# Performance work log

Hardware: AMD Instinct MI355X
Metric: run time of the kernel (lower is better)

Reference implementation:

```python
import jax, jax.numpy as jnp
import numpy as np

N, T, P = 8192, 2048, 24  # batch of series, time steps, seasonal period


def setup_inputs() -> dict:
    key = jax.random.key(0)
    k1, k2, k3, k4, k5, k6, k7 = jax.random.split(key, 7)
    return {
        "temp": jax.random.normal(k1, (N, T), dtype=jnp.float32),
        "alpha": jax.random.uniform(k2, (1,), dtype=jnp.float32),
        "beta": jax.random.uniform(k3, (1,), dtype=jnp.float32),
        "gamma": jax.random.uniform(k4, (1,), dtype=jnp.float32),
        "L0": jax.random.normal(k5, (N,), dtype=jnp.float32),
        "b0": jax.random.normal(k6, (N,), dtype=jnp.float32),
        "S0": jax.random.normal(k7, (N, P), dtype=jnp.float32),
        "seasonp": P,
    }


def reference(temp, alpha, beta, gamma, L0, b0, S0, seasonp):
    # Holt-Winters exponential smoothing recurrence (add trend), batched over N series.
    a, bt, g = alpha[0], beta[0], gamma[0]
    Tn = temp.shape[1]
    phases = jnp.arange(1, Tn, dtype=jnp.int32) % seasonp  # i % seasonp
    xs = temp[:, 1:].T  # [T-1, N]

    def step(carry, inp):
        L, b, buf = carry          # L,b: [N]; buf: [N, P] rolling seasonal buffer
        x, ph = inp
        s_read = buf[:, ph]        # S[i % seasonp] (most recent value at this phase)
        Ln = a * (x - s_read) + (1.0 - a) * (L + b)
        bn = bt * (Ln - L) + (1.0 - bt) * b
        sn = g * (x - Ln) + (1.0 - g) * s_read
        buf = buf.at[:, ph].set(sn)
        return (Ln, bn, buf), (Ln, bn, sn)

    (_, _, _), (Ls, bs, Ss) = jax.lax.scan(step, (L0, b0, S0), (xs, phases))
    L = jnp.concatenate([L0[:, None], Ls.T], axis=1)   # [N, T]
    b = jnp.concatenate([b0[:, None], bs.T], axis=1)   # [N, T]
    S = jnp.concatenate([S0[:, 0:1], Ss.T], axis=1)    # [N, T]
    return (L + b) * S
```

## Files before the change

kernel.cpp:

```cpp
#include <hip/hip_runtime.h>


typedef float f32x4 __attribute__((ext_vector_type(4)));

#define ALOAD(DST, PTR, OFF) \
  asm volatile("global_load_dwordx4 %0, %1, off offset:" #OFF \
               : "=v"(DST) : "v"(PTR));

#define ASTORE(PTR, VAL) \
  asm volatile("global_store_dwordx4 %0, %1, off" :: "v"(PTR), "v"(VAL));

#define WAITVM(N) \
  { asm volatile("s_waitcnt vmcnt(" #N ")" ::: "memory"); \
    __builtin_amdgcn_sched_barrier(0); }

__global__ __launch_bounds__(64, 1) void hw_kernel(
    const float* __restrict__ temp,
    const float* __restrict__ alpha,
    const float* __restrict__ beta,
    const float* __restrict__ gamma,
    const float* __restrict__ L0,
    const float* __restrict__ b0,
    const float* __restrict__ S0,
    float* __restrict__ out,
    int N, int T)
{
    __shared__ float ot[2][16 * 52];

    const int lane = threadIdx.x;
    const int row0 = blockIdx.x * 16;
    const int r    = lane & 15;
    const int row  = row0 + r;
    const bool l16 = (lane < 16);
    const float* xrow = temp + (size_t)row * T;

    f32x4 A0,A1,A2,A3,A4,A5,A6,A7,A8,A9,A10,A11;
    f32x4 B0,B1,B2,B3,B4,B5,B6,B7,B8,B9,B10,B11;

#define ISSUE12(Xp, P) { \
  ALOAD(Xp##0,(P),0)    ALOAD(Xp##1,(P),16)   ALOAD(Xp##2,(P),32)  \
  ALOAD(Xp##3,(P),48)   ALOAD(Xp##4,(P),64)   ALOAD(Xp##5,(P),80)  \
  ALOAD(Xp##6,(P),96)   ALOAD(Xp##7,(P),112)  ALOAD(Xp##8,(P),128) \
  ALOAD(Xp##9,(P),144)  ALOAD(Xp##10,(P),160) ALOAD(Xp##11,(P),176) }
#define ISSUE8(Xp, P) { \
  ALOAD(Xp##0,(P),0)    ALOAD(Xp##1,(P),16)   ALOAD(Xp##2,(P),32)  \
  ALOAD(Xp##3,(P),48)   ALOAD(Xp##4,(P),64)   ALOAD(Xp##5,(P),80)  \
  ALOAD(Xp##6,(P),96)   ALOAD(Xp##7,(P),112) }

    ISSUE12(A, xrow)
    ISSUE12(B, xrow + 48)
    const float* vaddr = xrow + 96;

    const float a_  = alpha[0];
    const float bt  = beta[0];
    const float g_  = gamma[0];
    const float oma = 1.0f - a_;
    const float omb = 1.0f - bt;
    const float opb = 1.0f + bt;

    float buf[24];
    {
        const float* s0r = S0 + (size_t)row * 24;
        #pragma unroll
        for (int p = 0; p < 6; ++p) {
            const f32x4 v = *reinterpret_cast<const f32x4*>(s0r + 4*p);
            buf[4*p]=v.x; buf[4*p+1]=v.y; buf[4*p+2]=v.z; buf[4*p+3]=v.w;
        }
    }
    float L = L0[row];
    float c = L + b0[row];
    float og[4] = {0.f, 0.f, 0.f, 0.f};

#define GSTEP(Q, E, XE) { \
    const float x_ = (XE); \
    const float s_ = buf[(4*(Q)+(E)) % 24]; \
    const float d_ = x_ - s_; \
    const float Ln = fmaf(oma, c, a_ * d_); \
    const float t1 = fmaf(omb, c, -L); \
    const float cn = fmaf(opb, Ln, t1); \
    const float sn = fmaf(g_, d_ - Ln, s_); \
    buf[(4*(Q)+(E)) % 24] = sn; \
    og[(E)] = cn * sn; \
    L = Ln; c = cn; }

#define GROUP(Q, XV, P) { \
    GSTEP(Q,0,(XV).x) GSTEP(Q,1,(XV).y) GSTEP(Q,2,(XV).z) GSTEP(Q,3,(XV).w) \
    if (l16) *reinterpret_cast<f32x4*>(&ot[P][r*52 + 4*(Q)]) = \
        (f32x4){og[0],og[1],og[2],og[3]}; }

#define WINCOMP_A(P) { GROUP(0,A0,P) GROUP(1,A1,P) GROUP(2,A2,P) GROUP(3,A3,P) \
    GROUP(4,A4,P) GROUP(5,A5,P) GROUP(6,A6,P) GROUP(7,A7,P) GROUP(8,A8,P) \
    GROUP(9,A9,P) GROUP(10,A10,P) GROUP(11,A11,P) }
#define WINCOMP_B(P) { GROUP(0,B0,P) GROUP(1,B1,P) GROUP(2,B2,P) GROUP(3,B3,P) \
    GROUP(4,B4,P) GROUP(5,B5,P) GROUP(6,B6,P) GROUP(7,B7,P) GROUP(8,B8,P) \
    GROUP(9,B9,P) GROUP(10,B10,P) GROUP(11,B11,P) }

    const int dr = lane >> 2;
    const int dc = lane & 3;
    float* obase = out + (size_t)(row0 + dr) * T + 4*dc;

#define DRAIN1(P, J) { \
    const f32x4 v_ = *reinterpret_cast<const f32x4*>( \
        &ot[P][dr*52 + 16*(J) + 4*dc]); \
    ASTORE(obase + 16*(J), v_); }

#define DRAIN(P) { DRAIN1(P,0) DRAIN1(P,1) DRAIN1(P,2) obase += 48; }

    WAITVM(12)
    {
        og[0] = c * buf[0];
        GSTEP(0,1,A0.y) GSTEP(0,2,A0.z) GSTEP(0,3,A0.w)
        if (l16) *reinterpret_cast<f32x4*>(&ot[0][r*52]) =
            (f32x4){og[0],og[1],og[2],og[3]};
    }
    GROUP(1,A1,0)  GROUP(2,A2,0)  GROUP(3,A3,0)  GROUP(4,A4,0)
    GROUP(5,A5,0)  GROUP(6,A6,0)  GROUP(7,A7,0)  GROUP(8,A8,0)
    GROUP(9,A9,0)  GROUP(10,A10,0) GROUP(11,A11,0)

    const int pairs = (T / 48 - 2) / 2;
    for (int h = 0; h < pairs; ++h) {
        ISSUE12(A, vaddr)
        vaddr += 48;
        DRAIN(0)
        WAITVM(15)
        WINCOMP_B(1)
        ISSUE12(B, vaddr)
        vaddr += 48;
        DRAIN(1)
        WAITVM(15)
        WINCOMP_A(0)
    }

    ISSUE8(A, vaddr)
    DRAIN(0)
    WAITVM(11)
    WINCOMP_B(1)

    DRAIN(1)
    WAITVM(6)
    GROUP(0,A0,0) GROUP(1,A1,0) GROUP(2,A2,0) GROUP(3,A3,0)
    GROUP(4,A4,0) GROUP(5,A5,0) GROUP(6,A6,0) GROUP(7,A7,0)
    DRAIN1(0,0) DRAIN1(0,1)

#undef GSTEP
#undef GROUP
#undef WINCOMP_A
#undef WINCOMP_B
#undef DRAIN1
#undef DRAIN
#undef ISSUE12
#undef ISSUE8
}

extern "C" void kernel_launch(void* const* d_in, const int* in_sizes, int n_in,
                              void* d_out, int out_size, void* d_ws, size_t ws_size,
                              hipStream_t stream) {
    const float* temp  = (const float*)d_in[0];
    const float* alpha = (const float*)d_in[1];
    const float* beta  = (const float*)d_in[2];
    const float* gamma = (const float*)d_in[3];
    const float* L0    = (const float*)d_in[4];
    const float* b0    = (const float*)d_in[5];
    const float* S0    = (const float*)d_in[6];
    float* out = (float*)d_out;

    const int N = in_sizes[4];
    const int T = in_sizes[0] / N;

    const int grid = (N + 15) / 16;
    hw_kernel<<<grid, 64, 0, stream>>>(
        temp, alpha, beta, gamma, L0, b0, S0, out, N, T);
}
```

Measured before the change: 53.30 us.

## Stage input tiles through LDS with coalesced row-wide loads and stores

Instead of each lane loading its own row in 48-element chunks held in registers, the wave now loads 240-column tiles of all 16 rows cooperatively. Each lane fetches 16 bytes per row, so a row segment is one contiguous access. The tiles go into a double-buffered LDS region, and the recurrence reads from LDS. Outputs are also written back row-wide from a 240-column LDS tile. This is meant to improve global memory coalescing and cut per-lane strided traffic, at the cost of extra LDS traffic, a full vmcnt(0) wait per tile and larger shared memory.

```diff
diff --git a/kernel.cpp b/kernel.cpp
--- a/kernel.cpp
+++ b/kernel.cpp
@@ -3,16 +3,16 @@
 
 typedef float f32x4 __attribute__((ext_vector_type(4)));
 
-#define ALOAD(DST, PTR, OFF) \
-  asm volatile("global_load_dwordx4 %0, %1, off offset:" #OFF \
-               : "=v"(DST) : "v"(PTR));
-
+#define ALOAD(DST, PTR) \
+  asm volatile("global_load_dwordx4 %0, %1, off" : "=v"(DST) : "v"(PTR));
 #define ASTORE(PTR, VAL) \
   asm volatile("global_store_dwordx4 %0, %1, off" :: "v"(PTR), "v"(VAL));
-
-#define WAITVM(N) \
-  { asm volatile("s_waitcnt vmcnt(" #N ")" ::: "memory"); \
+#define WAITVM0 \
+  { asm volatile("s_waitcnt vmcnt(0)" ::: "memory"); \
     __builtin_amdgcn_sched_barrier(0); }
+
+#define ROWD  244
+#define TILED (16 * ROWD)
 
 __global__ __launch_bounds__(64, 1) void hw_kernel(
     const float* __restrict__ temp,
@@ -25,38 +25,44 @@
     float* __restrict__ out,
     int N, int T)
 {
-    __shared__ float ot[2][16 * 52];
+    __shared__ __align__(16) float xs[2 * TILED];
+    __shared__ __align__(16) float ot[TILED];
 
     const int lane = threadIdx.x;
     const int row0 = blockIdx.x * 16;
     const int r    = lane & 15;
     const int row  = row0 + r;
-    const bool l16 = (lane < 16);
-    const float* xrow = temp + (size_t)row * T;
-
-    f32x4 A0,A1,A2,A3,A4,A5,A6,A7,A8,A9,A10,A11;
-    f32x4 B0,B1,B2,B3,B4,B5,B6,B7,B8,B9,B10,B11;
-
-#define ISSUE12(Xp, P) { \
-  ALOAD(Xp##0,(P),0)    ALOAD(Xp##1,(P),16)   ALOAD(Xp##2,(P),32)  \
-  ALOAD(Xp##3,(P),48)   ALOAD(Xp##4,(P),64)   ALOAD(Xp##5,(P),80)  \
-  ALOAD(Xp##6,(P),96)   ALOAD(Xp##7,(P),112)  ALOAD(Xp##8,(P),128) \
-  ALOAD(Xp##9,(P),144)  ALOAD(Xp##10,(P),160) ALOAD(Xp##11,(P),176) }
-#define ISSUE8(Xp, P) { \
-  ALOAD(Xp##0,(P),0)    ALOAD(Xp##1,(P),16)   ALOAD(Xp##2,(P),32)  \
-  ALOAD(Xp##3,(P),48)   ALOAD(Xp##4,(P),64)   ALOAD(Xp##5,(P),80)  \
-  ALOAD(Xp##6,(P),96)   ALOAD(Xp##7,(P),112) }
-
-    ISSUE12(A, xrow)
-    ISSUE12(B, xrow + 48)
-    const float* vaddr = xrow + 96;
-
-    const float a_  = alpha[0];
-    const float bt  = beta[0];
-    const float g_  = gamma[0];
-    const float oma = 1.0f - a_;
-    const float omb = 1.0f - bt;
-    const float opb = 1.0f + bt;
+
+    const float* gld = temp + (size_t)row0 * T + 4 * lane;
+    float*       gst = out  + (size_t)row0 * T + 4 * lane;
+
+    f32x4 G0,G1,G2,G3,G4,G5,G6,G7,G8,G9,G10,G11,G12,G13,G14,G15;
+
+#define ISSUE(CB, WDT) { if (4*lane < (WDT)) { \
+    const float* q_ = gld + (CB); \
+    ALOAD(G0 ,q_) q_ += T; ALOAD(G1 ,q_) q_ += T; ALOAD(G2 ,q_) q_ += T; \
+    ALOAD(G3 ,q_) q_ += T; ALOAD(G4 ,q_) q_ += T; ALOAD(G5 ,q_) q_ += T; \
+    ALOAD(G6 ,q_) q_ += T; ALOAD(G7 ,q_) q_ += T; ALOAD(G8 ,q_) q_ += T; \
+    ALOAD(G9 ,q_) q_ += T; ALOAD(G10,q_) q_ += T; ALOAD(G11,q_) q_ += T; \
+    ALOAD(G12,q_) q_ += T; ALOAD(G13,q_) q_ += T; ALOAD(G14,q_) q_ += T; \
+    ALOAD(G15,q_) } }
+
+#define STAGE(SEL, WDT) { if (4*lane < (WDT)) { \
+    float* w_ = xs + (SEL)*TILED + 4*lane; \
+    *(f32x4*)(w_+ 0*ROWD)=G0;  *(f32x4*)(w_+ 1*ROWD)=G1;  \
+    *(f32x4*)(w_+ 2*ROWD)=G2;  *(f32x4*)(w_+ 3*ROWD)=G3;  \
+    *(f32x4*)(w_+ 4*ROWD)=G4;  *(f32x4*)(w_+ 5*ROWD)=G5;  \
+    *(f32x4*)(w_+ 6*ROWD)=G6;  *(f32x4*)(w_+ 7*ROWD)=G7;  \
+    *(f32x4*)(w_+ 8*ROWD)=G8;  *(f32x4*)(w_+ 9*ROWD)=G9;  \
+    *(f32x4*)(w_+10*ROWD)=G10; *(f32x4*)(w_+11*ROWD)=G11; \
+    *(f32x4*)(w_+12*ROWD)=G12; *(f32x4*)(w_+13*ROWD)=G13; \
+    *(f32x4*)(w_+14*ROWD)=G14; *(f32x4*)(w_+15*ROWD)=G15; } }
+
+    const int wdt0 = (T < 240) ? T : 240;
+    ISSUE(0, wdt0)
+
+    const float a_ = alpha[0], bt = beta[0], g_ = gamma[0];
+    const float oma = 1.0f - a_, omb = 1.0f - bt, opb = 1.0f + bt;
 
     float buf[24];
     {
@@ -69,87 +75,132 @@
     }
     float L = L0[row];
     float c = L + b0[row];
-    float og[4] = {0.f, 0.f, 0.f, 0.f};
-
-#define GSTEP(Q, E, XE) { \
+    float og0, og1, og2, og3;
+
+    WAITVM0
+    STAGE(0, wdt0)
+
+#define GSTEPE(G_, E_, XE) { \
     const float x_ = (XE); \
-    const float s_ = buf[(4*(Q)+(E)) % 24]; \
+    const float s_ = buf[4*(G_)+(E_)]; \
     const float d_ = x_ - s_; \
     const float Ln = fmaf(oma, c, a_ * d_); \
     const float t1 = fmaf(omb, c, -L); \
     const float cn = fmaf(opb, Ln, t1); \
     const float sn = fmaf(g_, d_ - Ln, s_); \
-    buf[(4*(Q)+(E)) % 24] = sn; \
-    og[(E)] = cn * sn; \
+    buf[4*(G_)+(E_)] = sn; \
+    og##E_ = cn * sn; \
     L = Ln; c = cn; }
 
-#define GROUP(Q, XV, P) { \
-    GSTEP(Q,0,(XV).x) GSTEP(Q,1,(XV).y) GSTEP(Q,2,(XV).z) GSTEP(Q,3,(XV).w) \
-    if (l16) *reinterpret_cast<f32x4*>(&ot[P][r*52 + 4*(Q)]) = \
-        (f32x4){og[0],og[1],og[2],og[3]}; }
-
-#define WINCOMP_A(P) { GROUP(0,A0,P) GROUP(1,A1,P) GROUP(2,A2,P) GROUP(3,A3,P) \
-    GROUP(4,A4,P) GROUP(5,A5,P) GROUP(6,A6,P) GROUP(7,A7,P) GROUP(8,A8,P) \
-    GROUP(9,A9,P) GROUP(10,A10,P) GROUP(11,A11,P) }
-#define WINCOMP_B(P) { GROUP(0,B0,P) GROUP(1,B1,P) GROUP(2,B2,P) GROUP(3,B3,P) \
-    GROUP(4,B4,P) GROUP(5,B5,P) GROUP(6,B6,P) GROUP(7,B7,P) GROUP(8,B8,P) \
-    GROUP(9,B9,P) GROUP(10,B10,P) GROUP(11,B11,P) }
-
-    const int dr = lane >> 2;
-    const int dc = lane & 3;
-    float* obase = out + (size_t)(row0 + dr) * T + 4*dc;
-
-#define DRAIN1(P, J) { \
-    const f32x4 v_ = *reinterpret_cast<const f32x4*>( \
-        &ot[P][dr*52 + 16*(J) + 4*dc]); \
-    ASTORE(obase + 16*(J), v_); }
-
-#define DRAIN(P) { DRAIN1(P,0) DRAIN1(P,1) DRAIN1(P,2) obase += 48; }
-
-    WAITVM(12)
-    {
-        og[0] = c * buf[0];
-        GSTEP(0,1,A0.y) GSTEP(0,2,A0.z) GSTEP(0,3,A0.w)
-        if (l16) *reinterpret_cast<f32x4*>(&ot[0][r*52]) =
-            (f32x4){og[0],og[1],og[2],og[3]};
+#define GROUP(G_, XV, OFFD) { \
+    GSTEPE(G_,0,(XV).x) GSTEPE(G_,1,(XV).y) GSTEPE(G_,2,(XV).z) GSTEPE(G_,3,(XV).w) \
+    if (lane < 16) *reinterpret_cast<f32x4*>(otr + (OFFD) + 4*(G_)) = \
+        (f32x4){og0,og1,og2,og3}; }
+
+    const int NW = T / 240;
+
+    for (int k = 0; k < NW; ++k) {
+        const int cb = 240 * (k + 1);
+        int wdt = T - cb; if (wdt > 240) wdt = 240;
+        ISSUE(cb, wdt)
+
+        const float* xb  = xs + (k & 1) * TILED + r * ROWD;
+        float*       otr = ot + r * ROWD;
+
+        for (int cc = 0; cc < 10; ++cc) {
+            const int od = 24 * cc;
+            const f32x4 v0 = *reinterpret_cast<const f32x4*>(xb + od);
+            const f32x4 v1 = *reinterpret_cast<const f32x4*>(xb + od + 4);
+            const f32x4 v2 = *reinterpret_cast<const f32x4*>(xb + od + 8);
+            const f32x4 v3 = *reinterpret_cast<const f32x4*>(xb + od + 12);
+            const f32x4 v4 = *reinterpret_cast<const f32x4*>(xb + od + 16);
+            const f32x4 v5 = *reinterpret_cast<const f32x4*>(xb + od + 20);
+            if (k == 0 && cc == 0) {
+                og0 = c * buf[0];
+                GSTEPE(0,1,v0.y) GSTEPE(0,2,v0.z) GSTEPE(0,3,v0.w)
+                if (lane < 16) *reinterpret_cast<f32x4*>(otr) =
+                    (f32x4){og0,og1,og2,og3};
+            } else {
+                GROUP(0, v0, od)
+            }
+            GROUP(1, v1, od) GROUP(2, v2, od) GROUP(3, v3, od)
+            GROUP(4, v4, od) GROUP(5, v5, od)
+        }
+
+        WAITVM0
+        STAGE((k & 1) ^ 1, wdt)
+
+        if (lane < 60) {
+            const float* o2 = ot + 4 * lane;
+            float* q_ = gst + 240 * k;
+            f32x4 d_;
+            d_=*(const f32x4*)(o2+ 0*ROWD); ASTORE(q_,d_) q_+=T;
+            d_=*(const f32x4*)(o2+ 1*ROWD); ASTORE(q_,d_) q_+=T;
+            d_=*(const f32x4*)(o2+ 2*ROWD); ASTORE(q_,d_) q_+=T;
+            d_=*(const f32x4*)(o2+ 3*ROWD); ASTORE(q_,d_) q_+=T;
+            d_=*(const f32x4*)(o2+ 4*ROWD); ASTORE(q_,d_) q_+=T;
+            d_=*(const f32x4*)(o2+ 5*ROWD); ASTORE(q_,d_) q_+=T;
+            d_=*(const f32x4*)(o2+ 6*ROWD); ASTORE(q_,d_) q_+=T;
+            d_=*(const f32x4*)(o2+ 7*ROWD); ASTORE(q_,d_) q_+=T;
+            d_=*(const f32x4*)(o2+ 8*ROWD); ASTORE(q_,d_) q_+=T;
+            d_=*(const f32x4*)(o2+ 9*ROWD); ASTORE(q_,d_) q_+=T;
+            d_=*(const f32x4*)(o2+10*ROWD); ASTORE(q_,d_) q_+=T;
+            d_=*(const f32x4*)(o2+11*ROWD); ASTORE(q_,d_) q_+=T;
+            d_=*(const f32x4*)(o2+12*ROWD); ASTORE(q_,d_) q_+=T;
+            d_=*(const f32x4*)(o2+13*ROWD); ASTORE(q_,d_) q_+=T;
+            d_=*(const f32x4*)(o2+14*ROWD); ASTORE(q_,d_) q_+=T;
+            d_=*(const f32x4*)(o2+15*ROWD); ASTORE(q_,d_)
+        }
     }
-    GROUP(1,A1,0)  GROUP(2,A2,0)  GROUP(3,A3,0)  GROUP(4,A4,0)
-    GROUP(5,A5,0)  GROUP(6,A6,0)  GROUP(7,A7,0)  GROUP(8,A8,0)
-    GROUP(9,A9,0)  GROUP(10,A10,0) GROUP(11,A11,0)
-
-    const int pairs = (T / 48 - 2) / 2;
-    for (int h = 0; h < pairs; ++h) {
-        ISSUE12(A, vaddr)
-        vaddr += 48;
-        DRAIN(0)
-        WAITVM(15)
-        WINCOMP_B(1)
-        ISSUE12(B, vaddr)
-        vaddr += 48;
-        DRAIN(1)
-        WAITVM(15)
-        WINCOMP_A(0)
+
+    const int TB  = 240 * NW;
+    const int rem = T - TB;
+    if (rem > 0) {
+        const float* xb  = xs + (NW & 1) * TILED + r * ROWD;
+        float*       otr = ot + r * ROWD;
+        for (int cc = 0; 24 * cc < rem; ++cc) {
+            const int od = 24 * cc;
+            const int tb2 = TB + od;
+            const f32x4 v0 = *reinterpret_cast<const f32x4*>(xb + od);
+            const f32x4 v1 = *reinterpret_cast<const f32x4*>(xb + od + 4);
+            const f32x4 v2 = *reinterpret_cast<const f32x4*>(xb + od + 8);
+            const f32x4 v3 = *reinterpret_cast<const f32x4*>(xb + od + 12);
+            const f32x4 v4 = *reinterpret_cast<const f32x4*>(xb + od + 16);
+            const f32x4 v5 = *reinterpret_cast<const f32x4*>(xb + od + 20);
+            if (tb2 +  0 < T) { GROUP(0, v0, od) }
+            if (tb2 +  4 < T) { GROUP(1, v1, od) }
+            if (tb2 +  8 < T) { GROUP(2, v2, od) }
+            if (tb2 + 12 < T) { GROUP(3, v3, od) }
+            if (tb2 + 16 < T) { GROUP(4, v4, od) }
+            if (tb2 + 20 < T) { GROUP(5, v5, od) }
+        }
+        if (4 * lane < rem) {
+            const float* o2 = ot + 4 * lane;
+            float* q_ = gst + TB;
+            f32x4 d_;
+            d_=*(const f32x4*)(o2+ 0*ROWD); ASTORE(q_,d_) q_+=T;
+            d_=*(const f32x4*)(o2+ 1*ROWD); ASTORE(q_,d_) q_+=T;
+            d_=*(const f32x4*)(o2+ 2*ROWD); ASTORE(q_,d_) q_+=T;
+            d_=*(const f32x4*)(o2+ 3*ROWD); ASTORE(q_,d_) q_+=T;
+            d_=*(const f32x4*)(o2+ 4*ROWD); ASTORE(q_,d_) q_+=T;
+            d_=*(const f32x4*)(o2+ 5*ROWD); ASTORE(q_,d_) q_+=T;
+            d_=*(const f32x4*)(o2+ 6*ROWD); ASTORE(q_,d_) q_+=T;
+            d_=*(const f32x4*)(o2+ 7*ROWD); ASTORE(q_,d_) q_+=T;
+            d_=*(const f32x4*)(o2+ 8*ROWD); ASTORE(q_,d_) q_+=T;
+            d_=*(const f32x4*)(o2+ 9*ROWD); ASTORE(q_,d_) q_+=T;
+            d_=*(const f32x4*)(o2+10*ROWD); ASTORE(q_,d_) q_+=T;
+            d_=*(const f32x4*)(o2+11*ROWD); ASTORE(q_,d_) q_+=T;
+            d_=*(const f32x4*)(o2+12*ROWD); ASTORE(q_,d_) q_+=T;
+            d_=*(const f32x4*)(o2+13*ROWD); ASTORE(q_,d_) q_+=T;
+            d_=*(const f32x4*)(o2+14*ROWD); ASTORE(q_,d_) q_+=T;
+            d_=*(const f32x4*)(o2+15*ROWD); ASTORE(q_,d_)
+        }
     }
 
-    ISSUE8(A, vaddr)
-    DRAIN(0)
-    WAITVM(11)
-    WINCOMP_B(1)
-
-    DRAIN(1)
-    WAITVM(6)
-    GROUP(0,A0,0) GROUP(1,A1,0) GROUP(2,A2,0) GROUP(3,A3,0)
-    GROUP(4,A4,0) GROUP(5,A5,0) GROUP(6,A6,0) GROUP(7,A7,0)
-    DRAIN1(0,0) DRAIN1(0,1)
-
-#undef GSTEP
+#undef GSTEPE
 #undef GROUP
-#undef WINCOMP_A
-#undef WINCOMP_B
-#undef DRAIN1
-#undef DRAIN
-#undef ISSUE12
-#undef ISSUE8
+#undef ISSUE
+#undef STAGE
 }
 
 extern "C" void kernel_launch(void* const* d_in, const int* in_sizes, int n_in,
```

Result: slower. 62.54 us (+17.3%).
